# Kernel optimization log

Measured on AMD Instinct MI355X. Metric: run time of the kernel, lower is better.

The kernel has to match this reference:

```python
import math
import jax
import jax.numpy as jnp
import numpy as np

SEGMENT_SIZE = 2048   # w (init: segment_size)
DILATION_RATE = 4     # r (init: dilation_rate)
D_MODEL = 1024        # init: d_model


def _sparse_indices(n: int, w: int, r: int, head_idx: int) -> np.ndarray:
    """Static SparsifyIndices: per segment of size w, take tokens offset::r.
    Since r divides w, every segment yields exactly m=w//r indices (no -1 pad).
    Returns flat global token indices, shape (S*m,)."""
    S = n // w
    m = w // r
    off = head_idx % r
    seg_start = np.arange(S, dtype=np.int64)[:, None] * w      # (S,1)
    within = off + r * np.arange(m, dtype=np.int64)[None, :]   # (1,m)
    return (seg_start + within).reshape(-1)


def setup_inputs() -> dict:
    key = jax.random.key(0)
    x = jax.random.normal(key, (4, 8192, D_MODEL), dtype=jnp.float32)
    return {"x": x, "head_idx": 1}


def reference(x, head_idx):
    b, n0, d = x.shape
    w, r = SEGMENT_SIZE, DILATION_RATE
    pad = (-n0) % w
    if pad:
        x = jnp.pad(x, ((0, 0), (0, pad), (0, 0)))
    n = n0 + pad
    idx = _sparse_indices(n, w, r, int(head_idx))  # static, (S*m,)
    S, m = n // w, w // r

    # Gather dilated tokens per segment: (b, S, m, d)
    xg = x[:, idx, :].reshape(b, S, m, d)

    # Softmax attention within each sub-segment (q=k=v=xg)
    scores = jnp.einsum('bsid,bsjd->bsij', xg, xg) / math.sqrt(d)  # (b,S,m,m)
    probs = jax.nn.softmax(scores, axis=-1)
    att = jnp.einsum('bsij,bsjd->bsid', probs, xg).reshape(b, S * m, d)

    # MixOutputs: alpha-weighted scatter-add back to full sequence
    denoms = att.sum(-1)                                       # (b, S*m)
    denom_sums = jnp.zeros((b, n), x.dtype).at[:, idx].add(denoms)
    alphas = denoms / denom_sums[:, idx]                       # (b, S*m)
    out = jnp.zeros((b, n, d), x.dtype).at[:, idx, :].add(att * alphas[..., None])
    return out
```

## Files before the change

kernel.cpp:

```cpp
#include <hip/hip_runtime.h>
#include <hip/hip_bf16.h>


typedef __bf16 bf16_t;
typedef __bf16 bf16x8 __attribute__((ext_vector_type(8)));
typedef float floatx4 __attribute__((ext_vector_type(4)));

#define D_MODEL 1024
#define SEG_W   2048
#define RATE    4
#define M_SUB   512
#define NTOK    8192
#define NSEGT   16
#define XG_ELEMS ((long)NSEGT * M_SUB * D_MODEL)

__device__ __forceinline__ void gload16(const bf16_t* g, bf16_t* l) {
    __builtin_amdgcn_global_load_lds(
        (const __attribute__((address_space(1))) void*)g,
        (__attribute__((address_space(3))) void*)l, 16, 0, 0);
}

#define MFMA16(a, b, c) __builtin_amdgcn_mfma_f32_16x16x32_bf16((a), (b), (c), 0, 0, 0)

__device__ __forceinline__ void vwait(int n) {
    switch (n) {
    case 0:  asm volatile("s_waitcnt vmcnt(0)"  ::: "memory"); break;
    case 4:  asm volatile("s_waitcnt vmcnt(4)"  ::: "memory"); break;
    case 6:  asm volatile("s_waitcnt vmcnt(6)"  ::: "memory"); break;
    case 8:  asm volatile("s_waitcnt vmcnt(8)"  ::: "memory"); break;
    case 10: asm volatile("s_waitcnt vmcnt(10)" ::: "memory"); break;
    case 12: asm volatile("s_waitcnt vmcnt(12)" ::: "memory"); break;
    case 14: asm volatile("s_waitcnt vmcnt(14)" ::: "memory"); break;
    }
}

__global__ __launch_bounds__(256) void gather_kernel(
    const float* __restrict__ x, const int* __restrict__ hidp,
    bf16_t* __restrict__ xg, bf16_t* __restrict__ xgT)
{
    const int off = ((hidp[0] % RATE) + RATE) % RATE;
    const int bid = blockIdx.x;
    const int seg = bid >> 7;
    const int rem = bid & 127;
    const int it  = rem >> 4;
    const int dt  = rem & 15;
    const int b   = seg >> 2, s = seg & 3;

    __shared__ ushort tile[64][65];

    const int t  = threadIdx.x;
    const int r  = t >> 2;
    const int cq = (t & 3) << 4;

    union U8 { bf16x8 v; ushort u[8]; };

    {
        const int  i   = it * 64 + r;
        const long tok = (long)s * SEG_W + off + 4L * i;
        const float* src = x + ((long)b * NTOK + tok) * D_MODEL + dt * 64 + cq;
        float4 f0 = ((const float4*)src)[0];
        float4 f1 = ((const float4*)src)[1];
        float4 f2 = ((const float4*)src)[2];
        float4 f3 = ((const float4*)src)[3];
        U8 lo, hi;
        lo.v[0]=(bf16_t)f0.x; lo.v[1]=(bf16_t)f0.y; lo.v[2]=(bf16_t)f0.z; lo.v[3]=(bf16_t)f0.w;
        lo.v[4]=(bf16_t)f1.x; lo.v[5]=(bf16_t)f1.y; lo.v[6]=(bf16_t)f1.z; lo.v[7]=(bf16_t)f1.w;
        hi.v[0]=(bf16_t)f2.x; hi.v[1]=(bf16_t)f2.y; hi.v[2]=(bf16_t)f2.z; hi.v[3]=(bf16_t)f2.w;
        hi.v[4]=(bf16_t)f3.x; hi.v[5]=(bf16_t)f3.y; hi.v[6]=(bf16_t)f3.z; hi.v[7]=(bf16_t)f3.w;
        bf16_t* dstg = xg + ((long)seg * M_SUB + i) * D_MODEL + dt * 64 + cq;
        *(bf16x8*)(dstg)     = lo.v;
        *(bf16x8*)(dstg + 8) = hi.v;
        #pragma unroll
        for (int j = 0; j < 8; ++j) { tile[r][cq + j] = lo.u[j]; tile[r][cq + 8 + j] = hi.u[j]; }
    }
    __syncthreads();
    {
        const int dc = r;
        const int iq = cq;
        U8 o0, o1;
        #pragma unroll
        for (int j = 0; j < 8; ++j) { o0.u[j] = tile[iq + j][dc]; o1.u[j] = tile[iq + 8 + j][dc]; }
        bf16_t* dstT = xgT + ((long)seg * D_MODEL + dt * 64 + dc) * M_SUB + it * 64 + iq;
        *(bf16x8*)(dstT)     = o0.v;
        *(bf16x8*)(dstT + 8) = o1.v;
    }
}

__global__ __launch_bounds__(512, 2) void attn_kernel(
    const bf16_t* __restrict__ xg, const bf16_t* __restrict__ xgT,
    const int* __restrict__ hidp, float* __restrict__ out)
{
    const int off  = ((hidp[0] % RATE) + RATE) % RATE;
    const int bid0 = blockIdx.x;
    const int sub  = bid0 >> 3;
    const int seg  = (bid0 & 7) * 2 + (sub >> 4);
    const int band = sub & 15;
    const int b = seg >> 2, s = seg & 3;

    const int tid  = threadIdx.x;
    const int w    = tid >> 6;
    const int lane = tid & 63;
    const int l16  = lane & 15;
    const int quad = lane >> 4;

    __shared__ alignas(16) char arena[133120];
    bf16_t* Kring = (bf16_t*)arena;
    float (*redmax)[32] = (float(*)[32])(arena + 131072);
    float (*redsum)[32] = (float(*)[32])(arena + 132096);
    bf16_t* Pl    = (bf16_t*)arena;
    bf16_t* Vring = (bf16_t*)(arena + 32768);

    const bf16_t* xs = xg + (long)seg * M_SUB * D_MODEL;
    float* obase = out + (long)b * NTOK * D_MODEL;

    const bf16_t* qr0 = xs + (long)(band * 32 + l16) * D_MODEL + quad * 8;
    const bf16_t* qr1 = qr0 + 16 * D_MODEL;

    const bf16_t* ksrc = xs + (long)(w * 64 + (lane >> 2)) * D_MODEL
                            + (((lane & 3) ^ (lane >> 4)) * 8);
    auto stageK = [&](int buf, int t) {
        bf16_t* dst = Kring + buf * 16384 + (w * 64) * 32;
        const bf16_t* src = ksrc + t * 32;
        #pragma unroll
        for (int j = 0; j < 4; ++j)
            gload16(src + j * 16 * D_MODEL, dst + j * 512);
    };

    const bf16_t* vsrc = xgT + ((long)seg * D_MODEL + w * 64 + (lane >> 2)) * M_SUB
                             + (((lane & 3) ^ (lane >> 4)) * 8);
    auto stageV = [&](int buf, int t) {
        bf16_t* dst = Vring + buf * 16384 + (w * 64) * 32;
        const bf16_t* src = vsrc + (long)(t >> 4) * 512 * M_SUB + (t & 15) * 32;
        #pragma unroll
        for (int j = 0; j < 4; ++j)
            gload16(src + j * 16 * M_SUB, dst + j * 512);
    };

    auto zstore = [&](int t) {
        const floatx4 z = {0.f, 0.f, 0.f, 0.f};
        const int r2 = tid >> 7;
        const int j  = t * 4 + r2;
        const int q  = j / 3, e = j - 3 * (j / 3);
        const int delta = e + (e >= off ? 1 : 0);
        const long tok = (long)s * SEG_W + 4L * (band * 32 + q) + delta;
        float* dst = obase + tok * D_MODEL + (tid & 127) * 4;
        __builtin_nontemporal_store(z, (floatx4*)dst);
        __builtin_nontemporal_store(z, (floatx4*)(dst + 512));
    };

    const int rsw = (l16 >> 2) & 3;

    floatx4 accS[2][4];
    #pragma unroll
    for (int m = 0; m < 2; ++m)
        #pragma unroll
        for (int n = 0; n < 4; ++n) accS[m][n] = (floatx4){0.f, 0.f, 0.f, 0.f};

    bf16x8 qf[4][2];
    #pragma unroll
    for (int p0 = 0; p0 < 3; ++p0) {
        qf[p0][0] = *(const bf16x8*)(qr0 + p0 * 32);
        qf[p0][1] = *(const bf16x8*)(qr1 + p0 * 32);
        stageK(p0, p0);
    }

    #pragma unroll
    for (int t = 0; t < 32; ++t) {
        if (t <= 29)      vwait(12);
        else if (t == 30) vwait(6);
        else              vwait(0);

        const bf16_t* Kb = Kring + (t & 3) * 16384;
        bf16x8 Bf[4];
        #pragma unroll
        for (int n = 0; n < 4; ++n) {
            const int row = w * 64 + n * 16 + l16;
            Bf[n] = *(const bf16x8*)&Kb[row * 32 + ((quad ^ rsw) * 8)];
        }
        if (t <= 28) {
            qf[(t + 3) & 3][0] = *(const bf16x8*)(qr0 + (t + 3) * 32);
            qf[(t + 3) & 3][1] = *(const bf16x8*)(qr1 + (t + 3) * 32);
            stageK((t + 3) & 3, t + 3);
        }
        __builtin_amdgcn_s_setprio(1);
        #pragma unroll
        for (int n = 0; n < 4; ++n) {
            accS[0][n] = MFMA16(qf[t & 3][0], Bf[n], accS[0][n]);
            accS[1][n] = MFMA16(qf[t & 3][1], Bf[n], accS[1][n]);
        }
        __builtin_amdgcn_s_setprio(0);
    }

    #pragma unroll
    for (int m = 0; m < 2; ++m)
        #pragma unroll
        for (int n = 0; n < 4; ++n)
            #pragma unroll
            for (int rg = 0; rg < 4; ++rg) accS[m][n][rg] *= 0.03125f;

    float mx[2][4];
    #pragma unroll
    for (int m = 0; m < 2; ++m)
        #pragma unroll
        for (int rg = 0; rg < 4; ++rg)
            mx[m][rg] = fmaxf(fmaxf(accS[m][0][rg], accS[m][1][rg]),
                              fmaxf(accS[m][2][rg], accS[m][3][rg]));
    #pragma unroll
    for (int d = 1; d < 16; d <<= 1)
        #pragma unroll
        for (int m = 0; m < 2; ++m)
            #pragma unroll
            for (int rg = 0; rg < 4; ++rg)
                mx[m][rg] = fmaxf(mx[m][rg], __shfl_xor(mx[m][rg], d, 64));
    if (l16 == 0) {
        #pragma unroll
        for (int m = 0; m < 2; ++m)
            #pragma unroll
            for (int rg = 0; rg < 4; ++rg)
                redmax[w][m * 16 + quad * 4 + rg] = mx[m][rg];
    }
    __syncthreads();
    float gm[2][4];
    #pragma unroll
    for (int m = 0; m < 2; ++m)
        #pragma unroll
        for (int rg = 0; rg < 4; ++rg) {
            const int row = m * 16 + quad * 4 + rg;
            float g = redmax[0][row];
            #pragma unroll
            for (int ww = 1; ww < 8; ++ww) g = fmaxf(g, redmax[ww][row]);
            gm[m][rg] = g;
        }
    float sm[2][4] = {{0.f,0.f,0.f,0.f},{0.f,0.f,0.f,0.f}};
    #pragma unroll
    for (int m = 0; m < 2; ++m)
        #pragma unroll
        for (int n = 0; n < 4; ++n)
            #pragma unroll
            for (int rg = 0; rg < 4; ++rg) {
                const float e = __expf(accS[m][n][rg] - gm[m][rg]);
                accS[m][n][rg] = e;
                sm[m][rg] += e;
            }
    #pragma unroll
    for (int d = 1; d < 16; d <<= 1)
        #pragma unroll
        for (int m = 0; m < 2; ++m)
            #pragma unroll
            for (int rg = 0; rg < 4; ++rg)
                sm[m][rg] += __shfl_xor(sm[m][rg], d, 64);
    if (l16 == 0) {
        #pragma unroll
        for (int m = 0; m < 2; ++m)
            #pragma unroll
            for (int rg = 0; rg < 4; ++rg)
                redsum[w][m * 16 + quad * 4 + rg] = sm[m][rg];
    }
    __syncthreads();
    float iv[2][4];
    #pragma unroll
    for (int m = 0; m < 2; ++m)
        #pragma unroll
        for (int rg = 0; rg < 4; ++rg) {
            const int row = m * 16 + quad * 4 + rg;
            float tt = redsum[0][row];
            #pragma unroll
            for (int ww = 1; ww < 8; ++ww) tt += redsum[ww][row];
            iv[m][rg] = 1.f / tt;
        }

    stageV(0, 0); stageV(1, 1); stageV(2, 2);

    #pragma unroll
    for (int m = 0; m < 2; ++m)
        #pragma unroll
        for (int rg = 0; rg < 4; ++rg) {
            const int row = m * 16 + quad * 4 + rg;
            const float f = iv[m][rg];
            #pragma unroll
            for (int n = 0; n < 4; ++n) {
                const int col = w * 64 + n * 16 + l16;
                const int sw  = (((col >> 3) ^ (row & 7)) << 3) + (col & 7);
                Pl[row * 512 + sw] = (bf16_t)(accS[m][n][rg] * f);
            }
        }
    asm volatile("s_waitcnt lgkmcnt(0)" ::: "memory");
    __builtin_amdgcn_s_barrier();
    __builtin_amdgcn_sched_barrier(0);

    floatx4 accA[2][4], accB[2][4];
    #pragma unroll
    for (int m = 0; m < 2; ++m)
        #pragma unroll
        for (int n = 0; n < 4; ++n) {
            accA[m][n] = (floatx4){0.f, 0.f, 0.f, 0.f};
            accB[m][n] = (floatx4){0.f, 0.f, 0.f, 0.f};
        }

    #pragma unroll
    for (int t = 0; t < 32; ++t) {
        if      (t == 0)  vwait(8);
        else if (t == 1)  vwait(10);
        else if (t == 2)  vwait(12);
        else if (t <= 24) vwait(14);
        else if (t == 25) vwait(12);
        else if (t == 26) vwait(10);
        else if (t <= 29) vwait(8);
        else if (t == 30) vwait(4);
        else              vwait(0);

        const bf16_t* Vb = Vring + (t % 3) * 16384;
        bf16x8 Af[2], Bf[4];
        const int ch = ((t & 15) * 4 + quad) ^ (l16 & 7);
        #pragma unroll
        for (int m = 0; m < 2; ++m)
            Af[m] = *(const bf16x8*)&Pl[(m * 16 + l16) * 512 + ch * 8];
        #pragma unroll
        for (int n = 0; n < 4; ++n) {
            const int row = w * 64 + n * 16 + l16;
            Bf[n] = *(const bf16x8*)&Vb[row * 32 + ((quad ^ rsw) * 8)];
        }
        __builtin_amdgcn_s_setprio(1);
        if (t < 16) {
            #pragma unroll
            for (int n = 0; n < 4; ++n) {
                accA[0][n] = MFMA16(Af[0], Bf[n], accA[0][n]);
                accA[1][n] = MFMA16(Af[1], Bf[n], accA[1][n]);
            }
        } else {
            #pragma unroll
            for (int n = 0; n < 4; ++n) {
                accB[0][n] = MFMA16(Af[0], Bf[n], accB[0][n]);
                accB[1][n] = MFMA16(Af[1], Bf[n], accB[1][n]);
            }
        }
        __builtin_amdgcn_s_setprio(0);
        __builtin_amdgcn_sched_barrier(0);
        if (t <= 28) stageV((t + 3) % 3, t + 3);
        __builtin_amdgcn_sched_barrier(0);
        if (t <= 23) zstore(t);
    }

    #pragma unroll
    for (int m = 0; m < 2; ++m)
        #pragma unroll
        for (int rg = 0; rg < 4; ++rg) {
            const long tok = (long)s * SEG_W + off + 4L * (band * 32 + m * 16 + quad * 4 + rg);
            float* orow = obase + tok * D_MODEL;
            #pragma unroll
            for (int n = 0; n < 4; ++n) {
                const int d = w * 64 + n * 16 + l16;
                __builtin_nontemporal_store(accA[m][n][rg], orow + d);
                __builtin_nontemporal_store(accB[m][n][rg], orow + 512 + d);
            }
        }
}

extern "C" void kernel_launch(void* const* d_in, const int* in_sizes, int n_in,
                              void* d_out, int out_size, void* d_ws, size_t ws_size,
                              hipStream_t stream) {
    const float* x   = (const float*)d_in[0];
    const int*   hid = (const int*)d_in[1];
    float*       out = (float*)d_out;
    bf16_t* xg  = (bf16_t*)d_ws;
    bf16_t* xgT = xg + XG_ELEMS;

    gather_kernel<<<dim3(2048), dim3(256), 0, stream>>>(x, hid, xg, xgT);
    attn_kernel<<<dim3(256), dim3(512), 0, stream>>>(xg, xgT, hid, out);
}
```

Baseline: 243.0 us.

## Spread zero-fill stores across QK loop and overlap accA output stores with PV

```diff
diff --git a/kernel.cpp b/kernel.cpp
--- a/kernel.cpp
+++ b/kernel.cpp
@@ -25,12 +25,18 @@
 __device__ __forceinline__ void vwait(int n) {
     switch (n) {
     case 0:  asm volatile("s_waitcnt vmcnt(0)"  ::: "memory"); break;
-    case 4:  asm volatile("s_waitcnt vmcnt(4)"  ::: "memory"); break;
+    case 3:  asm volatile("s_waitcnt vmcnt(3)"  ::: "memory"); break;
     case 6:  asm volatile("s_waitcnt vmcnt(6)"  ::: "memory"); break;
     case 8:  asm volatile("s_waitcnt vmcnt(8)"  ::: "memory"); break;
+    case 9:  asm volatile("s_waitcnt vmcnt(9)"  ::: "memory"); break;
     case 10: asm volatile("s_waitcnt vmcnt(10)" ::: "memory"); break;
+    case 11: asm volatile("s_waitcnt vmcnt(11)" ::: "memory"); break;
     case 12: asm volatile("s_waitcnt vmcnt(12)" ::: "memory"); break;
+    case 13: asm volatile("s_waitcnt vmcnt(13)" ::: "memory"); break;
     case 14: asm volatile("s_waitcnt vmcnt(14)" ::: "memory"); break;
+    case 15: asm volatile("s_waitcnt vmcnt(15)" ::: "memory"); break;
+    case 16: asm volatile("s_waitcnt vmcnt(16)" ::: "memory"); break;
+    case 17: asm volatile("s_waitcnt vmcnt(17)" ::: "memory"); break;
     }
 }
 
@@ -136,16 +142,14 @@
             gload16(src + j * 16 * M_SUB, dst + j * 512);
     };
 
-    auto zstore = [&](int t) {
+    auto zstore = [&](int j0) {
         const floatx4 z = {0.f, 0.f, 0.f, 0.f};
-        const int r2 = tid >> 7;
-        const int j  = t * 4 + r2;
-        const int q  = j / 3, e = j - 3 * (j / 3);
+        const int j = j0 + (tid >> 8);
+        const int q = j / 3, e = j - 3 * (j / 3);
         const int delta = e + (e >= off ? 1 : 0);
         const long tok = (long)s * SEG_W + 4L * (band * 32 + q) + delta;
-        float* dst = obase + tok * D_MODEL + (tid & 127) * 4;
+        float* dst = obase + tok * D_MODEL + (tid & 255) * 4;
         __builtin_nontemporal_store(z, (floatx4*)dst);
-        __builtin_nontemporal_store(z, (floatx4*)(dst + 512));
     };
 
     const int rsw = (l16 >> 2) & 3;
@@ -166,9 +170,12 @@
 
     #pragma unroll
     for (int t = 0; t < 32; ++t) {
-        if (t <= 29)      vwait(12);
-        else if (t == 30) vwait(6);
-        else              vwait(0);
+        if      (t <= 8)  vwait(12);
+        else if (t == 9)  vwait(13);
+        else if (t == 10) vwait(14);
+        else if (t <= 29) vwait(15);
+        else if (t == 30) vwait(9);
+        else              vwait(3);
 
         const bf16_t* Kb = Kring + (t & 3) * 16384;
         bf16x8 Bf[4];
@@ -189,6 +196,8 @@
             accS[1][n] = MFMA16(qf[t & 3][1], Bf[n], accS[1][n]);
         }
         __builtin_amdgcn_s_setprio(0);
+        __builtin_amdgcn_sched_barrier(0);
+        if (t >= 8) zstore((t - 8) * 2);
     }
 
     #pragma unroll
@@ -300,14 +309,17 @@
     #pragma unroll
     for (int t = 0; t < 32; ++t) {
         if      (t == 0)  vwait(8);
-        else if (t == 1)  vwait(10);
-        else if (t == 2)  vwait(12);
-        else if (t <= 24) vwait(14);
-        else if (t == 25) vwait(12);
-        else if (t == 26) vwait(10);
-        else if (t <= 29) vwait(8);
-        else if (t == 30) vwait(4);
-        else              vwait(0);
+        else if (t == 1)  vwait(9);
+        else if (t == 2)  vwait(10);
+        else if (t <= 16) vwait(11);
+        else if (t == 17) vwait(13);
+        else if (t == 18) vwait(15);
+        else if (t <= 24) vwait(17);
+        else if (t == 25) vwait(16);
+        else if (t == 26) vwait(15);
+        else if (t <= 29) vwait(14);
+        else if (t == 30) vwait(10);
+        else              vwait(6);
 
         const bf16_t* Vb = Vring + (t % 3) * 16384;
         bf16x8 Af[2], Bf[4];
@@ -338,7 +350,20 @@
         __builtin_amdgcn_sched_barrier(0);
         if (t <= 28) stageV((t + 3) % 3, t + 3);
         __builtin_amdgcn_sched_barrier(0);
-        if (t <= 23) zstore(t);
+        if (t <= 23) zstore(48 + t * 2);
+        if (t >= 16) {
+            const int u = t - 16;
+            #pragma unroll
+            for (int vv = 0; vv < 2; ++vv) {
+                const int v  = u * 2 + vv;
+                const int m  = v >> 4, n = (v >> 2) & 3, rg = v & 3;
+                const long tok = (long)s * SEG_W + off
+                               + 4L * (band * 32 + m * 16 + quad * 4 + rg);
+                const int d = w * 64 + n * 16 + l16;
+                __builtin_nontemporal_store(accA[m][n][rg],
+                                            obase + tok * D_MODEL + d);
+            }
+        }
     }
 
     #pragma unroll
@@ -350,7 +375,6 @@
             #pragma unroll
             for (int n = 0; n < 4; ++n) {
                 const int d = w * 64 + n * 16 + l16;
-                __builtin_nontemporal_store(accA[m][n][rg], orow + d);
                 __builtin_nontemporal_store(accB[m][n][rg], orow + 512 + d);
             }
         }
```

Result: no change. 242.2 us (-0.3%).
